# Kernel tuning notes

Measured on AMD Instinct MI355X. Metric: run time of the kernel, lower is better.

Reference implementation:

```python
import jax, jax.numpy as jnp
import numpy as np

NUM_LAYERS = 2


def _lstm_scan(x, w_ih, w_hh):
    """x: [S,B,I]; w_ih: [4H,I]; w_hh: [4H,H]. Returns per-step (hs, cs): [S,B,H]."""
    S, B, _ = x.shape
    H = w_hh.shape[1]
    xg = jnp.einsum('sbi,gi->sbg', x, w_ih)  # precompute input contributions [S,B,4H]

    def step(carry, xg_t):
        h, c = carry
        gates = xg_t + h @ w_hh.T
        i, f, g, o = jnp.split(gates, 4, axis=-1)  # torch LSTM gate order
        i = jax.nn.sigmoid(i)
        f = jax.nn.sigmoid(f)
        g = jnp.tanh(g)
        o = jax.nn.sigmoid(o)
        c = f * c + i * g
        h = o * jnp.tanh(c)
        return (h, c), (h, c)

    init = (jnp.zeros((B, H), x.dtype), jnp.zeros((B, H), x.dtype))
    _, (hs, cs) = jax.lax.scan(step, init, xg)
    return hs, cs


def _stacked(x, w_ih, w_hh, reverse):
    """Stacked unidirectional LSTM. w_ih/w_hh: [L,4H,*].
    Returns (out [S,B,H], h_last [L,B,H], c_last [L,B,H]) matching stackedRNN
    semantics: for reverse, the returned 'last' hidden is the per-step state at
    original time index S-1 (first step processed in the reverse loop)."""
    h_last, c_last = [], []
    cur = x
    for layer in range(w_ih.shape[0]):
        xin = jnp.flip(cur, axis=0) if reverse else cur
        hs, cs = _lstm_scan(xin, w_ih[layer], w_hh[layer])
        if reverse:
            hs = jnp.flip(hs, axis=0)
            cs = jnp.flip(cs, axis=0)
        cur = hs
        h_last.append(hs[-1])  # faithful to torch code's layer[-1] indexing
        c_last.append(cs[-1])
    return cur, jnp.stack(h_last, 0), jnp.stack(c_last, 0)


def setup_inputs() -> dict:
    key = jax.random.key(0)
    ks = jax.random.split(key, 5)
    S, B, I, H, L = 256, 32, 1024, 1024, NUM_LAYERS
    stdev = 1.0 / np.sqrt(H)
    u = lambda k, shape: jax.random.uniform(k, shape, jnp.float32, -stdev, stdev)
    return {
        'x': jax.random.normal(ks[0], (S, B, I), jnp.float32),
        'w_ih_fwd': u(ks[1], (L, 4 * H, I)),
        'w_hh_fwd': u(ks[2], (L, 4 * H, H)),
        'w_ih_bwd': u(ks[3], (L, 4 * H, I)),
        'w_hh_bwd': u(ks[4], (L, 4 * H, H)),
    }


def reference(x, w_ih_fwd, w_hh_fwd, w_ih_bwd, w_hh_bwd):
    out_f, h_f, c_f = _stacked(x, w_ih_fwd, w_hh_fwd, reverse=False)
    out_b, h_b, c_b = _stacked(x, w_ih_bwd, w_hh_bwd, reverse=True)
    output = jnp.concatenate([out_f, out_b], axis=-1)      # [S,B,2H]
    h_all = jnp.concatenate([h_f, h_b], axis=-1)            # [L,B,2H]
    c_all = jnp.concatenate([c_f, c_b], axis=-1)            # [L,B,2H]
    return output, h_all, c_all
```

## Files before the change

kernel.cpp:

```cpp
#include <hip/hip_runtime.h>
#include <stdint.h>

#define SEQ   256
#define BSZ   32
#define HD    1024
#define GD    4096
#define KD    1024
#define MROWS (SEQ*BSZ)
#define PBLK  128
#define PTHR  512

typedef unsigned short u16;
typedef __attribute__((ext_vector_type(8))) __bf16 bf8_t;
typedef __attribute__((ext_vector_type(4))) float  f4_t;
typedef __attribute__((ext_vector_type(4))) unsigned int u4_t;

__device__ __forceinline__ u16 f2bf(float f) {
  unsigned u = __float_as_uint(f);
  u += 0x7fffu + ((u >> 16) & 1u);
  return (u16)(u >> 16);
}
__device__ __forceinline__ float bf2f(u16 s) {
  return __uint_as_float(((unsigned)s) << 16);
}
__device__ __forceinline__ void async_copy16(const void* g, void* l) {
  __builtin_amdgcn_global_load_lds(
      (const __attribute__((address_space(1))) void*)g,
      (__attribute__((address_space(3))) void*)l, 16, 0, 0);
}
__device__ __forceinline__ float sigm(float x) { return 1.0f / (1.0f + __expf(-x)); }
__device__ __forceinline__ float tanh_f(float x) {
  float e = __expf(-2.0f * x);
  return 2.0f / (1.0f + e) - 1.0f;
}

__global__ void cvt_f32_bf16(const float* __restrict__ src, u16* __restrict__ dst, int n4) {
  int i = blockIdx.x * blockDim.x + threadIdx.x;
  if (i >= n4) return;
  float4 v = ((const float4*)src)[i];
  ushort4 o;
  o.x = f2bf(v.x); o.y = f2bf(v.y); o.z = f2bf(v.z); o.w = f2bf(v.w);
  ((ushort4*)dst)[i] = o;
}

__global__ void reorder_whh(const float* __restrict__ src, u16* __restrict__ dst, int d) {
  int r = blockIdx.x;
  int layer = r >> 12, row = r & 4095;
  int g = row >> 10, j = row & 1023;
  int jblk = j >> 4, jl = j & 15;
  size_t drow = ((size_t)(d * 2 + layer) * 64 + jblk) * 64 + g * 16 + jl;
  float4 v = ((const float4*)(src + (size_t)r * KD))[threadIdx.x];
  ushort4 o;
  o.x = f2bf(v.x); o.y = f2bf(v.y); o.z = f2bf(v.z); o.w = f2bf(v.w);
  ((ushort4*)(dst + drow * KD))[threadIdx.x] = o;
}

__global__ __launch_bounds__(256) void gemm_bt(
    const u16* __restrict__ A, const u16* __restrict__ B, u16* __restrict__ C,
    int M, int N, int K)
{
  __shared__ u16 lA[128 * 32];
  __shared__ u16 lB[128 * 32];
  const int tid  = threadIdx.x;
  const int wave = tid >> 6, lane = tid & 63;
  const int wr = (wave >> 1) * 64, wc = (wave & 1) * 64;
  const int m0 = blockIdx.x * 128, n0 = blockIdx.y * 128;

  f4_t acc[4][4] = {};

  const int r0 = tid >> 2,          kp0 = (tid & 3) * 8;
  const int r1 = (tid + 256) >> 2,  kp1 = (tid & 3) * 8;
  const u16* gA0 = A + (size_t)(m0 + r0) * K + kp0;
  const u16* gA1 = A + (size_t)(m0 + r1) * K + kp1;
  const u16* gB0 = B + (size_t)(n0 + r0) * K + kp0;
  const u16* gB1 = B + (size_t)(n0 + r1) * K + kp1;
  u16* lA0 = lA + wave * 512;          u16* lA1 = lA + 2048 + wave * 512;
  u16* lB0 = lB + wave * 512;          u16* lB1 = lB + 2048 + wave * 512;

  const int fr = lane & 15, fk = (lane >> 4) * 8;

  for (int k0 = 0; k0 < K; k0 += 32) {
    async_copy16(gA0 + k0, lA0);
    async_copy16(gA1 + k0, lA1);
    async_copy16(gB0 + k0, lB0);
    async_copy16(gB1 + k0, lB1);
    __syncthreads();
    bf8_t af[4], bf[4];
    #pragma unroll
    for (int i = 0; i < 4; i++) af[i] = *(const bf8_t*)&lA[(wr + i * 16 + fr) * 32 + fk];
    #pragma unroll
    for (int i = 0; i < 4; i++) bf[i] = *(const bf8_t*)&lB[(wc + i * 16 + fr) * 32 + fk];
    #pragma unroll
    for (int mi = 0; mi < 4; mi++)
      #pragma unroll
      for (int ni = 0; ni < 4; ni++)
        acc[mi][ni] = __builtin_amdgcn_mfma_f32_16x16x32_bf16(af[mi], bf[ni], acc[mi][ni], 0, 0, 0);
    __syncthreads();
  }
  const int er = (lane >> 4) * 4, ec = lane & 15;
  #pragma unroll
  for (int mi = 0; mi < 4; mi++)
    #pragma unroll
    for (int ni = 0; ni < 4; ni++)
      #pragma unroll
      for (int r = 0; r < 4; r++) {
        int m = m0 + wr + mi * 16 + er + r;
        int n = n0 + wc + ni * 16 + ec;
        C[(size_t)m * N + n] = f2bf(acc[mi][ni][r]);
      }
}

__global__ __launch_bounds__(PTHR) void lstm_persist(
    const u16* __restrict__ whh_r,
    const u16* __restrict__ xg,
    u16*       __restrict__ hst,
    u16*       __restrict__ h0out,
    float*     __restrict__ dout,
    unsigned*  __restrict__ cnt,
    int layer)
{
  const int tid = threadIdx.x;
  const int lane = tid & 63;
  const int mt = (tid >> 6) >> 1, kh = (tid >> 6) & 1;
  const int d = blockIdx.x & 1, jblk = blockIdx.x >> 1;
  const int j0 = jblk * 16;
  const int fr = lane & 15, quad = lane >> 4;

  __shared__ __align__(16) uint32_t lH[32 * 512];
  float* lAcc = (float*)lH;

  u4_t wreg[16];
  {
    const u16* wp = whh_r
        + ((size_t)(((d * 2 + layer) * 64 + jblk) * 64 + mt * 16 + fr)) * KD
        + kh * 512 + quad * 8;
    #pragma unroll
    for (int ks = 0; ks < 16; ks++) wreg[ks] = *(const u4_t*)(wp + ks * 32);
    #pragma unroll
    for (int ks = 0; ks < 16; ks++) asm volatile("" : "+v"(wreg[ks]));
  }

  const int b_ = tid >> 3, jp = tid & 7;
  float cr0 = 0.0f, cr1 = 0.0f;

  for (int t = 0; t < SEQ; t++) {
    const int tt = d ? (SEQ - 1 - t) : t;
    const int rbuf = t & 1, wbuf = rbuf ^ 1;

    unsigned long long* hsrc = (unsigned long long*)(hst + (size_t)(rbuf * 2 + d) * BSZ * HD);
    unsigned long long hv[16];
    #pragma unroll
    for (int g = 0; g < 16; g++)
      hv[g] = __hip_atomic_load(hsrc + g * 512 + tid, __ATOMIC_RELAXED, __HIP_MEMORY_SCOPE_AGENT);

    uint32_t xv[4];
    if (tid < 256) {
      const uint32_t* xgp = (const uint32_t*)(xg
          + ((size_t)d * MROWS + (size_t)tt * BSZ + b_) * GD + j0) + jp;
      #pragma unroll
      for (int g = 0; g < 4; g++) xv[g] = xgp[g * 512];
    }

    #pragma unroll
    for (int g = 0; g < 16; g++) {
      int qi = g * 512 + tid;
      int row = qi >> 8, c8 = qi & 255;
      int chunk = (c8 >> 1) ^ (row & 7);
      *(unsigned long long*)&lH[row * 512 + chunk * 4 + (c8 & 1) * 2] = hv[g];
    }
    __syncthreads();

    f4_t acc0 = {}, acc1 = {};
    #pragma unroll
    for (int ks = 0; ks < 16; ks++) {
      int cbase = ((kh * 64 + ks * 4 + quad) ^ (fr & 7)) << 2;
      bf8_t a0 = *(const bf8_t*)&lH[fr * 512 + cbase];
      bf8_t a1 = *(const bf8_t*)&lH[(fr + 16) * 512 + cbase];
      bf8_t wb = __builtin_bit_cast(bf8_t, wreg[ks]);
      acc0 = __builtin_amdgcn_mfma_f32_16x16x32_bf16(a0, wb, acc0, 0, 0, 0);
      acc1 = __builtin_amdgcn_mfma_f32_16x16x32_bf16(a1, wb, acc1, 0, 0, 0);
    }
    __syncthreads();

    #pragma unroll
    for (int r = 0; r < 4; r++) {
      lAcc[((mt * 2 + kh) * 32 + quad * 4 + r) * 16 + fr]      = acc0[r];
      lAcc[((mt * 2 + kh) * 32 + 16 + quad * 4 + r) * 16 + fr] = acc1[r];
    }
    __syncthreads();

    if (tid < 256) {
      float vg0[4], vg1[4];
      #pragma unroll
      for (int g = 0; g < 4; g++) {
        float2 p0 = *(const float2*)&lAcc[((g * 2 + 0) * 32 + b_) * 16 + 2 * jp];
        float2 p1 = *(const float2*)&lAcc[((g * 2 + 1) * 32 + b_) * 16 + 2 * jp];
        vg0[g] = p0.x + p1.x + bf2f((u16)(xv[g] & 0xffffu));
        vg1[g] = p0.y + p1.y + bf2f((u16)(xv[g] >> 16));
      }
      float i0 = sigm(vg0[0]), f0 = sigm(vg0[1]), g0 = tanh_f(vg0[2]), o0 = sigm(vg0[3]);
      float i1 = sigm(vg1[0]), f1 = sigm(vg1[1]), g1 = tanh_f(vg1[2]), o1 = sigm(vg1[3]);
      cr0 = f0 * cr0 + i0 * g0;
      cr1 = f1 * cr1 + i1 * g1;
      float hn0 = o0 * tanh_f(cr0), hn1 = o1 * tanh_f(cr1);
      uint32_t hnp = ((uint32_t)f2bf(hn1) << 16) | (uint32_t)f2bf(hn0);

      size_t hq = (((size_t)(wbuf * 2 + d) * BSZ + b_) * HD + j0 + 2 * jp) >> 1;
      __hip_atomic_store((uint32_t*)hst + hq, hnp, __ATOMIC_RELAXED, __HIP_MEMORY_SCOPE_AGENT);

      if (layer == 0) {
        *(uint32_t*)&h0out[((size_t)d * MROWS + (size_t)tt * BSZ + b_) * HD + j0 + 2 * jp] = hnp;
      } else {
        float2 o2 = make_float2(hn0, hn1);
        *(float2*)&dout[((size_t)tt * BSZ + b_) * (2 * HD) + (size_t)d * HD + j0 + 2 * jp] = o2;
      }
      if ((d == 0 && t == SEQ - 1) || (d == 1 && t == 0)) {
        size_t hoff = (size_t)MROWS * 2 * HD + ((size_t)layer * BSZ + b_) * (2 * HD)
                    + (size_t)d * HD + j0 + 2 * jp;
        dout[hoff] = hn0;  dout[hoff + 1] = hn1;
        dout[hoff + (size_t)2 * BSZ * 2 * HD]     = cr0;
        dout[hoff + (size_t)2 * BSZ * 2 * HD + 1] = cr1;
      }
    }

    asm volatile("s_waitcnt vmcnt(0)" ::: "memory");
    __syncthreads();
    if (tid == 0) {
      const unsigned sub = (unsigned)(blockIdx.x & 7);
      unsigned old = __hip_atomic_fetch_add(&cnt[16 * (1 + sub)], 1u,
                                            __ATOMIC_RELAXED, __HIP_MEMORY_SCOPE_AGENT);
      if (old + 1u == (unsigned)(PBLK / 8) * (unsigned)(t + 1))
        __hip_atomic_fetch_add(&cnt[0], 1u, __ATOMIC_RELAXED, __HIP_MEMORY_SCOPE_AGENT);
      const unsigned goal = 8u * (unsigned)(t + 1);
      long spins = 0;
      while (__hip_atomic_load(&cnt[0], __ATOMIC_RELAXED, __HIP_MEMORY_SCOPE_AGENT) < goal) {
        if (++spins > (1L << 27)) break;
      }
    }
    __syncthreads();
    asm volatile("" ::: "memory");
  }
}

extern "C" void kernel_launch(void* const* d_in, const int* in_sizes, int n_in,
                              void* d_out, int out_size, void* d_ws, size_t ws_size,
                              hipStream_t stream) {
  const float* x    = (const float*)d_in[0];
  const float* wihf = (const float*)d_in[1];
  const float* whhf = (const float*)d_in[2];
  const float* wihb = (const float*)d_in[3];
  const float* whhb = (const float*)d_in[4];
  float* out = (float*)d_out;

  const size_t NE = (size_t)MROWS * KD;
  char* ws = (char*)d_ws;
  u16*   xbf  = (u16*)ws;
  u16*   wih  = (u16*)(ws + NE * 2);
  u16*   whhr = wih + 2 * NE;
  u16*   xg   = whhr + 2 * NE;
  u16*   h0   = xg + (size_t)2 * MROWS * GD;
  u16*   hst  = h0 + (size_t)2 * MROWS * HD;
  unsigned* cnt = (unsigned*)(hst + (size_t)2 * 2 * BSZ * HD);

  const int n4 = (int)(NE / 4);
  const int cg = n4 / 256;
  cvt_f32_bf16<<<cg, 256, 0, stream>>>(x,    xbf,      n4);
  cvt_f32_bf16<<<cg, 256, 0, stream>>>(wihf, wih,      n4);
  cvt_f32_bf16<<<cg, 256, 0, stream>>>(wihb, wih + NE, n4);
  reorder_whh<<<2 * GD, 256, 0, stream>>>(whhf, whhr, 0);
  reorder_whh<<<2 * GD, 256, 0, stream>>>(whhb, whhr, 1);

  hipMemsetAsync(cnt, 0, 2048, stream);
  const size_t hstBytes = (size_t)2 * 2 * BSZ * HD * 2;
  hipMemsetAsync(hst, 0, hstBytes, stream);

  dim3 gg(MROWS / 128, GD / 128);

  for (int d = 0; d < 2; d++)
    gemm_bt<<<gg, 256, 0, stream>>>(xbf, wih + (size_t)(d * 2) * GD * KD,
                                    xg + (size_t)d * MROWS * GD, MROWS, GD, KD);
  lstm_persist<<<PBLK, PTHR, 0, stream>>>(whhr, xg, hst, h0, out, cnt, 0);

  for (int d = 0; d < 2; d++)
    gemm_bt<<<gg, 256, 0, stream>>>(h0 + (size_t)d * MROWS * HD,
                                    wih + (size_t)(d * 2 + 1) * GD * KD,
                                    xg + (size_t)d * MROWS * GD, MROWS, GD, KD);
  hipMemsetAsync(hst, 0, hstBytes, stream);
  lstm_persist<<<PBLK, PTHR, 0, stream>>>(whhr, xg, hst, h0, out, cnt + 256, 1);
}
```

Before: 3.276 ms.

## Split LSTM grid barrier per direction and read h from trajectory buffer

The forward and backward directions now each sync on their own 64-block barrier counter instead of one shared 128-block barrier, so one direction no longer waits on the other. The double-buffered hidden-state scratch is removed. Each step reads the previous h directly from the layer's output trajectory with 128-bit loads, which drops a redundant store per step and the per-layer memsets. The recurrent matvec at t=0 is skipped because h is zero. The risk is that h is now read with plain loads, with only one acquire fence at kernel start, so visibility relies on each address being read only after the barrier.

```diff
diff --git a/kernel.cpp b/kernel.cpp
--- a/kernel.cpp
+++ b/kernel.cpp
@@ -113,10 +113,9 @@
 __global__ __launch_bounds__(PTHR) void lstm_persist(
     const u16* __restrict__ whh_r,
     const u16* __restrict__ xg,
-    u16*       __restrict__ hst,
-    u16*       __restrict__ h0out,
+    u16*       __restrict__ htraj,
     float*     __restrict__ dout,
-    unsigned*  __restrict__ cnt,
+    unsigned*  __restrict__ cntb,
     int layer)
 {
   const int tid = threadIdx.x;
@@ -125,6 +124,9 @@
   const int d = blockIdx.x & 1, jblk = blockIdx.x >> 1;
   const int j0 = jblk * 16;
   const int fr = lane & 15, quad = lane >> 4;
+  unsigned* cnt = cntb + (size_t)d * 512;
+
+  __builtin_amdgcn_fence(__ATOMIC_ACQUIRE, "agent");
 
   __shared__ __align__(16) uint32_t lH[32 * 512];
   float* lAcc = (float*)lH;
@@ -145,13 +147,6 @@
 
   for (int t = 0; t < SEQ; t++) {
     const int tt = d ? (SEQ - 1 - t) : t;
-    const int rbuf = t & 1, wbuf = rbuf ^ 1;
-
-    unsigned long long* hsrc = (unsigned long long*)(hst + (size_t)(rbuf * 2 + d) * BSZ * HD);
-    unsigned long long hv[16];
-    #pragma unroll
-    for (int g = 0; g < 16; g++)
-      hv[g] = __hip_atomic_load(hsrc + g * 512 + tid, __ATOMIC_RELAXED, __HIP_MEMORY_SCOPE_AGENT);
 
     uint32_t xv[4];
     if (tid < 256) {
@@ -161,42 +156,54 @@
       for (int g = 0; g < 4; g++) xv[g] = xgp[g * 512];
     }
 
-    #pragma unroll
-    for (int g = 0; g < 16; g++) {
-      int qi = g * 512 + tid;
-      int row = qi >> 8, c8 = qi & 255;
-      int chunk = (c8 >> 1) ^ (row & 7);
-      *(unsigned long long*)&lH[row * 512 + chunk * 4 + (c8 & 1) * 2] = hv[g];
-    }
-    __syncthreads();
-
-    f4_t acc0 = {}, acc1 = {};
-    #pragma unroll
-    for (int ks = 0; ks < 16; ks++) {
-      int cbase = ((kh * 64 + ks * 4 + quad) ^ (fr & 7)) << 2;
-      bf8_t a0 = *(const bf8_t*)&lH[fr * 512 + cbase];
-      bf8_t a1 = *(const bf8_t*)&lH[(fr + 16) * 512 + cbase];
-      bf8_t wb = __builtin_bit_cast(bf8_t, wreg[ks]);
-      acc0 = __builtin_amdgcn_mfma_f32_16x16x32_bf16(a0, wb, acc0, 0, 0, 0);
-      acc1 = __builtin_amdgcn_mfma_f32_16x16x32_bf16(a1, wb, acc1, 0, 0, 0);
-    }
-    __syncthreads();
-
-    #pragma unroll
-    for (int r = 0; r < 4; r++) {
-      lAcc[((mt * 2 + kh) * 32 + quad * 4 + r) * 16 + fr]      = acc0[r];
-      lAcc[((mt * 2 + kh) * 32 + 16 + quad * 4 + r) * 16 + fr] = acc1[r];
-    }
-    __syncthreads();
+    if (t > 0) {
+      const int ttp = d ? (tt + 1) : (tt - 1);
+      const u16* hsrc = htraj + ((size_t)d * MROWS + (size_t)ttp * BSZ) * HD;
+      u4_t hv[8];
+      #pragma unroll
+      for (int g = 0; g < 8; g++)
+        hv[g] = *(const u4_t*)(hsrc + (size_t)(g * 512 + tid) * 8);
+      #pragma unroll
+      for (int g = 0; g < 8; g++) {
+        int lc = g * 512 + tid;
+        int row = lc >> 7, c = lc & 127;
+        int pc = c ^ (row & 7);
+        *(u4_t*)&lH[row * 512 + pc * 4] = hv[g];
+      }
+      __syncthreads();
+
+      f4_t acc0 = {}, acc1 = {};
+      #pragma unroll
+      for (int ks = 0; ks < 16; ks++) {
+        int cbase = ((kh * 64 + ks * 4 + quad) ^ (fr & 7)) << 2;
+        bf8_t a0 = *(const bf8_t*)&lH[fr * 512 + cbase];
+        bf8_t a1 = *(const bf8_t*)&lH[(fr + 16) * 512 + cbase];
+        bf8_t wb = __builtin_bit_cast(bf8_t, wreg[ks]);
+        acc0 = __builtin_amdgcn_mfma_f32_16x16x32_bf16(a0, wb, acc0, 0, 0, 0);
+        acc1 = __builtin_amdgcn_mfma_f32_16x16x32_bf16(a1, wb, acc1, 0, 0, 0);
+      }
+      __syncthreads();
+
+      #pragma unroll
+      for (int r = 0; r < 4; r++) {
+        lAcc[((mt * 2 + kh) * 32 + quad * 4 + r) * 16 + fr]      = acc0[r];
+        lAcc[((mt * 2 + kh) * 32 + 16 + quad * 4 + r) * 16 + fr] = acc1[r];
+      }
+      __syncthreads();
+    }
 
     if (tid < 256) {
       float vg0[4], vg1[4];
       #pragma unroll
       for (int g = 0; g < 4; g++) {
-        float2 p0 = *(const float2*)&lAcc[((g * 2 + 0) * 32 + b_) * 16 + 2 * jp];
-        float2 p1 = *(const float2*)&lAcc[((g * 2 + 1) * 32 + b_) * 16 + 2 * jp];
-        vg0[g] = p0.x + p1.x + bf2f((u16)(xv[g] & 0xffffu));
-        vg1[g] = p0.y + p1.y + bf2f((u16)(xv[g] >> 16));
+        float s0 = 0.f, s1 = 0.f;
+        if (t > 0) {
+          float2 p0 = *(const float2*)&lAcc[((g * 2 + 0) * 32 + b_) * 16 + 2 * jp];
+          float2 p1 = *(const float2*)&lAcc[((g * 2 + 1) * 32 + b_) * 16 + 2 * jp];
+          s0 = p0.x + p1.x; s1 = p0.y + p1.y;
+        }
+        vg0[g] = s0 + bf2f((u16)(xv[g] & 0xffffu));
+        vg1[g] = s1 + bf2f((u16)(xv[g] >> 16));
       }
       float i0 = sigm(vg0[0]), f0 = sigm(vg0[1]), g0 = tanh_f(vg0[2]), o0 = sigm(vg0[3]);
       float i1 = sigm(vg1[0]), f1 = sigm(vg1[1]), g1 = tanh_f(vg1[2]), o1 = sigm(vg1[3]);
@@ -205,12 +212,10 @@
       float hn0 = o0 * tanh_f(cr0), hn1 = o1 * tanh_f(cr1);
       uint32_t hnp = ((uint32_t)f2bf(hn1) << 16) | (uint32_t)f2bf(hn0);
 
-      size_t hq = (((size_t)(wbuf * 2 + d) * BSZ + b_) * HD + j0 + 2 * jp) >> 1;
-      __hip_atomic_store((uint32_t*)hst + hq, hnp, __ATOMIC_RELAXED, __HIP_MEMORY_SCOPE_AGENT);
-
-      if (layer == 0) {
-        *(uint32_t*)&h0out[((size_t)d * MROWS + (size_t)tt * BSZ + b_) * HD + j0 + 2 * jp] = hnp;
-      } else {
+      size_t hq = (((size_t)d * MROWS + (size_t)tt * BSZ + b_) * HD + j0 + 2 * jp) >> 1;
+      __hip_atomic_store((uint32_t*)htraj + hq, hnp, __ATOMIC_RELAXED, __HIP_MEMORY_SCOPE_AGENT);
+
+      if (layer == 1) {
         float2 o2 = make_float2(hn0, hn1);
         *(float2*)&dout[((size_t)tt * BSZ + b_) * (2 * HD) + (size_t)d * HD + j0 + 2 * jp] = o2;
       }
@@ -226,10 +231,10 @@
     asm volatile("s_waitcnt vmcnt(0)" ::: "memory");
     __syncthreads();
     if (tid == 0) {
-      const unsigned sub = (unsigned)(blockIdx.x & 7);
+      const unsigned sub = (unsigned)((blockIdx.x >> 1) & 7);
       unsigned old = __hip_atomic_fetch_add(&cnt[16 * (1 + sub)], 1u,
                                             __ATOMIC_RELAXED, __HIP_MEMORY_SCOPE_AGENT);
-      if (old + 1u == (unsigned)(PBLK / 8) * (unsigned)(t + 1))
+      if (old + 1u == 8u * (unsigned)(t + 1))
         __hip_atomic_fetch_add(&cnt[0], 1u, __ATOMIC_RELAXED, __HIP_MEMORY_SCOPE_AGENT);
       const unsigned goal = 8u * (unsigned)(t + 1);
       long spins = 0;
@@ -259,8 +264,7 @@
   u16*   whhr = wih + 2 * NE;
   u16*   xg   = whhr + 2 * NE;
   u16*   h0   = xg + (size_t)2 * MROWS * GD;
-  u16*   hst  = h0 + (size_t)2 * MROWS * HD;
-  unsigned* cnt = (unsigned*)(hst + (size_t)2 * 2 * BSZ * HD);
+  unsigned* cnt = (unsigned*)(h0 + (size_t)2 * MROWS * HD);
 
   const int n4 = (int)(NE / 4);
   const int cg = n4 / 256;
@@ -270,21 +274,18 @@
   reorder_whh<<<2 * GD, 256, 0, stream>>>(whhf, whhr, 0);
   reorder_whh<<<2 * GD, 256, 0, stream>>>(whhb, whhr, 1);
 
-  hipMemsetAsync(cnt, 0, 2048, stream);
-  const size_t hstBytes = (size_t)2 * 2 * BSZ * HD * 2;
-  hipMemsetAsync(hst, 0, hstBytes, stream);
+  hipMemsetAsync(cnt, 0, 4 * 512 * sizeof(unsigned), stream);
 
   dim3 gg(MROWS / 128, GD / 128);
 
   for (int d = 0; d < 2; d++)
     gemm_bt<<<gg, 256, 0, stream>>>(xbf, wih + (size_t)(d * 2) * GD * KD,
                                     xg + (size_t)d * MROWS * GD, MROWS, GD, KD);
-  lstm_persist<<<PBLK, PTHR, 0, stream>>>(whhr, xg, hst, h0, out, cnt, 0);
+  lstm_persist<<<PBLK, PTHR, 0, stream>>>(whhr, xg, h0, out, cnt, 0);
 
   for (int d = 0; d < 2; d++)
     gemm_bt<<<gg, 256, 0, stream>>>(h0 + (size_t)d * MROWS * HD,
                                     wih + (size_t)(d * 2 + 1) * GD * KD,
                                     xg + (size_t)d * MROWS * GD, MROWS, GD, KD);
-  hipMemsetAsync(hst, 0, hstBytes, stream);
-  lstm_persist<<<PBLK, PTHR, 0, stream>>>(whhr, xg, hst, h0, out, cnt + 256, 1);
-}
+  lstm_persist<<<PBLK, PTHR, 0, stream>>>(whhr, xg, h0, out, cnt + 1024, 1);
+}
```

Result: faster. 2.975 ms (-9.2%).
